# Kernel optimization log

Hardware: AMD Instinct MI355X
Metric: run time of the kernel (lower is better)

## Reference

```python
import jax, jax.numpy as jnp
import numpy as np

H = 32        # num query heads
KVH = 8       # num kv heads (GQA)
D = 128       # head_size
DV = 128      # head_size_v
SCALE = 0.08838834764831845  # 1/sqrt(128)


def setup_inputs() -> dict:
    key = jax.random.key(0)
    k1, k2, k3 = jax.random.split(key, 3)
    T = 4096  # packed tokens: B=4 sequences of seq_len=1024
    return {
        "query": jax.random.normal(k1, (T, H * D), dtype=jnp.float32),
        "key": jax.random.normal(k2, (T, KVH * D), dtype=jnp.float32),
        "value": jax.random.normal(k3, (T, KVH * DV), dtype=jnp.float32),
        "seq_len": 1024,
    }


def reference(query, key, value, seq_len):
    # Packed varlen causal GQA attention: tokens [T, H*D] split into B
    # sequences of length seq_len, causal mask within each sequence.
    T = query.shape[0]
    B = T // seq_len
    G = H // KVH  # GQA group size

    q = query.reshape(B, seq_len, H, D)
    k = key.reshape(B, seq_len, KVH, D)
    v = value.reshape(B, seq_len, KVH, DV)

    # expand kv heads to match query heads (head i uses kv head i // G)
    k = jnp.repeat(k, G, axis=2)  # [B, S, H, D]
    v = jnp.repeat(v, G, axis=2)  # [B, S, H, DV]

    scores = jnp.einsum("bqhd,bkhd->bhqk", q, k) * SCALE  # [B, H, S, S]
    causal = jnp.tril(jnp.ones((seq_len, seq_len), dtype=bool))
    scores = jnp.where(causal[None, None], scores, jnp.finfo(scores.dtype).min)
    probs = jax.nn.softmax(scores, axis=-1)
    out = jnp.einsum("bhqk,bkhd->bqhd", probs, v)  # [B, S, H, DV]
    return out.reshape(T, H * DV)
```

## Files before the change

### kernel.cpp

```cpp
#include <hip/hip_runtime.h>
#include <hip/hip_bf16.h>

#define H_   32
#define KVH_ 8
#define D_   128
#define DV_  128
#define SEQ_ 1024
#define QKD  (H_*D_)
#define KVD  (KVH_*D_)
#define CS_  (0.08838834764831845f * 1.4426950408889634f)
#define MFIX 8.0f
#define VOFF 8388608

typedef __attribute__((ext_vector_type(8))) short bf16x8;
typedef __attribute__((ext_vector_type(8))) unsigned short u16x8;
typedef __attribute__((ext_vector_type(4))) float f32x4;
typedef __attribute__((ext_vector_type(4))) unsigned int u32x4;

typedef const __attribute__((address_space(1))) void* gp_t;
typedef __attribute__((address_space(3))) void* lp_t;

#if __has_builtin(__builtin_amdgcn_exp2f)
#define EXP2F(x) __builtin_amdgcn_exp2f(x)
#else
#define EXP2F(x) exp2f(x)
#endif

static __device__ __forceinline__ unsigned short f2b(float x) {
    __hip_bfloat16 b = __float2bfloat16(x);
    return __builtin_bit_cast(unsigned short, b);
}
static __device__ __forceinline__ unsigned pk2(float a, float b) {
    return (unsigned)f2b(a) | ((unsigned)f2b(b) << 16);
}

__global__ __launch_bounds__(256)
void prep_kv(const float* __restrict__ K, const float* __restrict__ V,
             unsigned short* __restrict__ Kb, unsigned short* __restrict__ Vt) {
    if (blockIdx.x < 2048) {
        const int gt = blockIdx.x * 256 + threadIdx.x;
        const int q  = gt & 15;
        const int r  = gt >> 4;
        const int s  = r & 1023;
        const int bh = r >> 10;
        const int b = bh >> 3, kvh = bh & 7;
        const float* src = K + ((size_t)(b * SEQ_ + s)) * KVD + kvh * D_ + q * 8;
        float4 a = *(const float4*)src;
        float4 c = *(const float4*)(src + 4);
        u32x4 o = { pk2(a.x, a.y), pk2(a.z, a.w), pk2(c.x, c.y), pk2(c.z, c.w) };
        *(u32x4*)(Kb + (size_t)r * 128 + q * 8) = o;
    } else {
        const int gt = (blockIdx.x - 2048) * 256 + threadIdx.x;
        const int dv = gt & 127;
        const int uc = (gt >> 7) & 127;
        const int bh = gt >> 14;
        const int b = bh >> 3, kvh = bh & 7;
        const int C  = uc * 8;
        const int t  = C >> 5;
        const float* src = V + ((size_t)(b * SEQ_)) * KVD + kvh * DV_ + dv;
        unsigned short e[8];
#pragma unroll
        for (int i = 0; i < 8; ++i) {
            const int c = (C & 31) + i;
            const int kl = 4 * ((c >> 3) & 3) + (c & 3) + 16 * ((c >> 2) & 1);
            const int s = (t << 5) + kl;
            e[i] = f2b(src[(size_t)s * KVD]);
        }
        u16x8 o = { e[0], e[1], e[2], e[3], e[4], e[5], e[6], e[7] };
        *(u16x8*)(Vt + ((size_t)bh * 128 + dv) * SEQ_ + C) = o;
    }
}

__global__ __launch_bounds__(512, 4)
void attn_fwd(const float* __restrict__ Q,
              const unsigned short* __restrict__ Kb,
              float* __restrict__ O) {
    __shared__ __align__(16) unsigned short KS[2][32 * 128];
    __shared__ __align__(16) unsigned short VT[2][128 * 32];

    const int raw = (int)blockIdx.x;
    const int qt  = 7 - (raw >> 7);
    const int low = raw & 127;
    const int kvh = low & 7;
    const int hq  = (low >> 3) & 3;
    const int b   = low >> 5;
    const int h   = kvh * 4 + hq;
    const int bh  = b * 8 + kvh;

    const int tid = threadIdx.x;
    const int w   = tid >> 6;
    const int l   = tid & 63;
    const int lo  = l & 15;
    const int g   = l >> 4;

    const int kr = tid >> 4, ks = tid & 15;
    const int offk = kr * 256 + (((ks & 8) | ((ks & 7) ^ (kr & 7))) << 4);
    const int offv = VOFF + (tid >> 2) * 2048 + (((tid & 3) ^ ((tid >> 3) & 3)) << 4);

    const char* base = (const char*)Kb + (size_t)bh * 262144;

    auto issue = [&](int t, int dsel) {
        char* ksd = (char*)KS[dsel] + w * 1024;
        char* vsd = (char*)VT[dsel] + w * 1024;
        __builtin_amdgcn_global_load_lds((gp_t)(base + (size_t)(offk + t * 8192)), (lp_t)ksd, 16, 0, 0);
        __builtin_amdgcn_global_load_lds((gp_t)(base + (size_t)(offv + t * 64)),   (lp_t)vsd, 16, 0, 0);
    };

    const int ntiles = 4 * qt + 4;
    const int qw0    = qt * 128 + w * 16;
    const int jmaxw  = (qw0 + 15) >> 5;

    const float* Qb = Q + ((size_t)(b * SEQ_ + qw0 + lo)) * QKD + h * D_;
    bf16x8 qf[4];
#pragma unroll
    for (int cc = 0; cc < 4; ++cc) {
        const float* qp = Qb + cc * 32 + g * 8;
        float4 x0 = *(const float4*)(qp);
        float4 x1 = *(const float4*)(qp + 4);
        bf16x8 f;
        f[0] = f2b(x0.x * CS_); f[1] = f2b(x0.y * CS_);
        f[2] = f2b(x0.z * CS_); f[3] = f2b(x0.w * CS_);
        f[4] = f2b(x1.x * CS_); f[5] = f2b(x1.y * CS_);
        f[6] = f2b(x1.z * CS_); f[7] = f2b(x1.w * CS_);
        qf[cc] = f;
    }

    float lsum = 0.f;
    f32x4 o_[8];
#pragma unroll
    for (int db = 0; db < 8; ++db) o_[db] = (f32x4){0.f, 0.f, 0.f, 0.f};

    issue(0, 0);

#pragma unroll 1
    for (int j = 0; j < ntiles; ++j) {
        __syncthreads();
        if (j + 1 < ntiles) issue(j + 1, (j + 1) & 1);
        if (j <= jmaxw) {
            const int k0 = j * 32;
            const int d  = j & 1;

            f32x4 s0 = (f32x4){0.f, 0.f, 0.f, 0.f};
            f32x4 s1 = (f32x4){0.f, 0.f, 0.f, 0.f};
            const int sw = (lo & 7) << 4;
            const char* kbase = (const char*)KS[d];
            __builtin_amdgcn_s_setprio(1);
#pragma unroll
            for (int cc = 0; cc < 4; ++cc) {
                bf16x8 kf0 = *(const bf16x8*)(kbase + ((lo * 256 + cc * 64 + g * 16) ^ sw));
                bf16x8 kf1 = *(const bf16x8*)(kbase + (((16 + lo) * 256 + cc * 64 + g * 16) ^ sw));
                s0 = __builtin_amdgcn_mfma_f32_16x16x32_bf16(kf0, qf[cc], s0, 0, 0, 0);
                s1 = __builtin_amdgcn_mfma_f32_16x16x32_bf16(kf1, qf[cc], s1, 0, 0, 0);
            }
            __builtin_amdgcn_s_setprio(0);

            const int q_  = qw0 + lo;
            const bool needmask = (k0 + 31) > qw0;
            float pp[8];
#pragma unroll
            for (int i = 0; i < 4; ++i) {
                float v0 = s0[i], v1 = s1[i];
                if (needmask) {
                    if (k0 + 4 * g + i > q_)      v0 = -INFINITY;
                    if (k0 + 16 + 4 * g + i > q_) v1 = -INFINITY;
                }
                pp[i]     = EXP2F(v0 - MFIX);
                pp[4 + i] = EXP2F(v1 - MFIX);
            }
            lsum += ((pp[0] + pp[1]) + (pp[2] + pp[3]))
                  + ((pp[4] + pp[5]) + (pp[6] + pp[7]));
            u32x4 pu = { pk2(pp[0], pp[1]), pk2(pp[2], pp[3]),
                         pk2(pp[4], pp[5]), pk2(pp[6], pp[7]) };
            bf16x8 pf = __builtin_bit_cast(bf16x8, pu);

            const char* vbase = (const char*)VT[d];
            const int swv = ((lo >> 1) & 3) << 4;
            __builtin_amdgcn_s_setprio(1);
#pragma unroll
            for (int db = 0; db < 8; ++db) {
                bf16x8 vf = *(const bf16x8*)(vbase + (db * 16 + lo) * 64 + ((g * 16) ^ swv));
                o_[db] = __builtin_amdgcn_mfma_f32_16x16x32_bf16(pf, vf, o_[db], 0, 0, 0);
            }
            __builtin_amdgcn_s_setprio(0);
        }
    }

    float rs = lsum;
    rs += __shfl_xor(rs, 16);
    rs += __shfl_xor(rs, 32);
#pragma unroll
    for (int i = 0; i < 4; ++i) {
        const float inv = 1.0f / __shfl(rs, 4 * g + i);
        float* op = O + ((size_t)(b * SEQ_ + qw0 + 4 * g + i)) * (H_ * DV_) + h * DV_ + lo;
#pragma unroll
        for (int db = 0; db < 8; ++db) op[db * 16] = o_[db][i] * inv;
    }
}

extern "C" void kernel_launch(void* const* d_in, const int* in_sizes, int n_in,
                              void* d_out, int out_size, void* d_ws, size_t ws_size,
                              hipStream_t stream) {
    const float* Q = (const float*)d_in[0];
    const float* K = (const float*)d_in[1];
    const float* V = (const float*)d_in[2];
    float* Out = (float*)d_out;
    unsigned short* Kb = (unsigned short*)d_ws;
    unsigned short* Vt = (unsigned short*)((char*)d_ws + VOFF);
    prep_kv<<<dim3(4096), dim3(256), 0, stream>>>(K, V, Kb, Vt);
    attn_fwd<<<dim3(1024), dim3(512), 0, stream>>>(Q, Kb, Out);
}
```

Baseline: 72.05 us.

## Double KV tile to 64 keys per iteration to halve barrier count

Each main-loop iteration now stages 64 keys of K and V into LDS instead of 32, and processes them as two 32-key sub-tiles. This halves the number of __syncthreads and async-load rounds per block, with a new V swizzle matching the wider row. LDS use doubles to 64 KB per block and the occupancy hint of 4 blocks is dropped, so fewer blocks may be resident per CU.

```diff
diff --git a/kernel.cpp b/kernel.cpp
--- a/kernel.cpp
+++ b/kernel.cpp
@@ -71,12 +71,12 @@
     }
 }
 
-__global__ __launch_bounds__(512, 4)
+__global__ __launch_bounds__(512)
 void attn_fwd(const float* __restrict__ Q,
               const unsigned short* __restrict__ Kb,
               float* __restrict__ O) {
-    __shared__ __align__(16) unsigned short KS[2][32 * 128];
-    __shared__ __align__(16) unsigned short VT[2][128 * 32];
+    __shared__ __align__(16) unsigned short KS[2][64 * 128];
+    __shared__ __align__(16) unsigned short VT[2][128 * 64];
 
     const int raw = (int)blockIdx.x;
     const int qt  = 7 - (raw >> 7);
@@ -93,22 +93,30 @@
     const int lo  = l & 15;
     const int g   = l >> 4;
 
-    const int kr = tid >> 4, ks = tid & 15;
-    const int offk = kr * 256 + (((ks & 8) | ((ks & 7) ^ (kr & 7))) << 4);
-    const int offv = VOFF + (tid >> 2) * 2048 + (((tid & 3) ^ ((tid >> 3) & 3)) << 4);
+    const int kr0 = tid >> 4, ks0 = tid & 15;
+    const int kr1 = kr0 + 32;
+    const int offk0 = kr0 * 256 + (((ks0 & 8) | ((ks0 & 7) ^ (kr0 & 7))) << 4);
+    const int offk1 = kr1 * 256 + (((ks0 & 8) | ((ks0 & 7) ^ (kr1 & 7))) << 4);
+    const int dv0 = tid >> 3, vi = tid & 7;
+    const int offv0 = VOFF + dv0 * 2048 + ((vi ^ (dv0 & 7)) << 4);
+    const int offv1 = VOFF + (dv0 + 64) * 2048 + ((vi ^ (dv0 & 7)) << 4);
 
     const char* base = (const char*)Kb + (size_t)bh * 262144;
 
     auto issue = [&](int t, int dsel) {
         char* ksd = (char*)KS[dsel] + w * 1024;
         char* vsd = (char*)VT[dsel] + w * 1024;
-        __builtin_amdgcn_global_load_lds((gp_t)(base + (size_t)(offk + t * 8192)), (lp_t)ksd, 16, 0, 0);
-        __builtin_amdgcn_global_load_lds((gp_t)(base + (size_t)(offv + t * 64)),   (lp_t)vsd, 16, 0, 0);
+        const int ko = t * 16384;
+        const int vo = t * 128;
+        __builtin_amdgcn_global_load_lds((gp_t)(base + (size_t)(offk0 + ko)), (lp_t)ksd,          16, 0, 0);
+        __builtin_amdgcn_global_load_lds((gp_t)(base + (size_t)(offk1 + ko)), (lp_t)(ksd + 8192), 16, 0, 0);
+        __builtin_amdgcn_global_load_lds((gp_t)(base + (size_t)(offv0 + vo)), (lp_t)vsd,          16, 0, 0);
+        __builtin_amdgcn_global_load_lds((gp_t)(base + (size_t)(offv1 + vo)), (lp_t)(vsd + 8192), 16, 0, 0);
     };
 
-    const int ntiles = 4 * qt + 4;
+    const int ntiles = 2 * qt + 2;
     const int qw0    = qt * 128 + w * 16;
-    const int jmaxw  = (qw0 + 15) >> 5;
+    const int jmaxw  = (qw0 + 15) >> 6;
 
     const float* Qb = Q + ((size_t)(b * SEQ_ + qw0 + lo)) * QKD + h * D_;
     bf16x8 qf[4];
@@ -137,51 +145,56 @@
         __syncthreads();
         if (j + 1 < ntiles) issue(j + 1, (j + 1) & 1);
         if (j <= jmaxw) {
-            const int k0 = j * 32;
-            const int d  = j & 1;
-
-            f32x4 s0 = (f32x4){0.f, 0.f, 0.f, 0.f};
-            f32x4 s1 = (f32x4){0.f, 0.f, 0.f, 0.f};
+            const int d = j & 1;
+            const char* kbase = (const char*)KS[d];
+            const char* vbase = (const char*)VT[d];
             const int sw = (lo & 7) << 4;
-            const char* kbase = (const char*)KS[d];
-            __builtin_amdgcn_s_setprio(1);
-#pragma unroll
-            for (int cc = 0; cc < 4; ++cc) {
-                bf16x8 kf0 = *(const bf16x8*)(kbase + ((lo * 256 + cc * 64 + g * 16) ^ sw));
-                bf16x8 kf1 = *(const bf16x8*)(kbase + (((16 + lo) * 256 + cc * 64 + g * 16) ^ sw));
-                s0 = __builtin_amdgcn_mfma_f32_16x16x32_bf16(kf0, qf[cc], s0, 0, 0, 0);
-                s1 = __builtin_amdgcn_mfma_f32_16x16x32_bf16(kf1, qf[cc], s1, 0, 0, 0);
+
+#pragma unroll
+            for (int sub = 0; sub < 2; ++sub) {
+                const int k0 = j * 64 + sub * 32;
+                if (k0 > qw0 + 15) continue;
+
+                f32x4 s0 = (f32x4){0.f, 0.f, 0.f, 0.f};
+                f32x4 s1 = (f32x4){0.f, 0.f, 0.f, 0.f};
+                const int krow = sub * 32;
+                __builtin_amdgcn_s_setprio(1);
+#pragma unroll
+                for (int cc = 0; cc < 4; ++cc) {
+                    bf16x8 kf0 = *(const bf16x8*)(kbase + (((krow + lo) * 256 + cc * 64 + g * 16) ^ sw));
+                    bf16x8 kf1 = *(const bf16x8*)(kbase + (((krow + 16 + lo) * 256 + cc * 64 + g * 16) ^ sw));
+                    s0 = __builtin_amdgcn_mfma_f32_16x16x32_bf16(kf0, qf[cc], s0, 0, 0, 0);
+                    s1 = __builtin_amdgcn_mfma_f32_16x16x32_bf16(kf1, qf[cc], s1, 0, 0, 0);
+                }
+                __builtin_amdgcn_s_setprio(0);
+
+                const int q_  = qw0 + lo;
+                const bool needmask = (k0 + 31) > qw0;
+                float pp[8];
+#pragma unroll
+                for (int i = 0; i < 4; ++i) {
+                    float v0 = s0[i], v1 = s1[i];
+                    if (needmask) {
+                        if (k0 + 4 * g + i > q_)      v0 = -INFINITY;
+                        if (k0 + 16 + 4 * g + i > q_) v1 = -INFINITY;
+                    }
+                    pp[i]     = EXP2F(v0 - MFIX);
+                    pp[4 + i] = EXP2F(v1 - MFIX);
+                }
+                lsum += ((pp[0] + pp[1]) + (pp[2] + pp[3]))
+                      + ((pp[4] + pp[5]) + (pp[6] + pp[7]));
+                u32x4 pu = { pk2(pp[0], pp[1]), pk2(pp[2], pp[3]),
+                             pk2(pp[4], pp[5]), pk2(pp[6], pp[7]) };
+                bf16x8 pf = __builtin_bit_cast(bf16x8, pu);
+
+                __builtin_amdgcn_s_setprio(1);
+#pragma unroll
+                for (int db = 0; db < 8; ++db) {
+                    bf16x8 vf = *(const bf16x8*)(vbase + (db * 16 + lo) * 128 + ((sub * 64 + g * 16) ^ sw));
+                    o_[db] = __builtin_amdgcn_mfma_f32_16x16x32_bf16(pf, vf, o_[db], 0, 0, 0);
+                }
+                __builtin_amdgcn_s_setprio(0);
             }
-            __builtin_amdgcn_s_setprio(0);
-
-            const int q_  = qw0 + lo;
-            const bool needmask = (k0 + 31) > qw0;
-            float pp[8];
-#pragma unroll
-            for (int i = 0; i < 4; ++i) {
-                float v0 = s0[i], v1 = s1[i];
-                if (needmask) {
-                    if (k0 + 4 * g + i > q_)      v0 = -INFINITY;
-                    if (k0 + 16 + 4 * g + i > q_) v1 = -INFINITY;
-                }
-                pp[i]     = EXP2F(v0 - MFIX);
-                pp[4 + i] = EXP2F(v1 - MFIX);
-            }
-            lsum += ((pp[0] + pp[1]) + (pp[2] + pp[3]))
-                  + ((pp[4] + pp[5]) + (pp[6] + pp[7]));
-            u32x4 pu = { pk2(pp[0], pp[1]), pk2(pp[2], pp[3]),
-                         pk2(pp[4], pp[5]), pk2(pp[6], pp[7]) };
-            bf16x8 pf = __builtin_bit_cast(bf16x8, pu);
-
-            const char* vbase = (const char*)VT[d];
-            const int swv = ((lo >> 1) & 3) << 4;
-            __builtin_amdgcn_s_setprio(1);
-#pragma unroll
-            for (int db = 0; db < 8; ++db) {
-                bf16x8 vf = *(const bf16x8*)(vbase + (db * 16 + lo) * 64 + ((g * 16) ^ swv));
-                o_[db] = __builtin_amdgcn_mfma_f32_16x16x32_bf16(pf, vf, o_[db], 0, 0, 0);
-            }
-            __builtin_amdgcn_s_setprio(0);
         }
     }
 
```

Measured after the change: 71.15 us. About the same (-1.2%).

## Switch attention to 32x32x16 MFMA with 4-wave blocks and pre-swizzled KV

Applied to the files above, without the earlier changes.

Reworks the attention kernel so each wave handles 32 query rows using 32x32x16 bf16 MFMA instead of 16x16x32, and halves the block to 256 threads. The KV prep kernel now writes K and V already in the swizzled tile order the kernel reads, so tile loads become contiguous global-to-LDS copies. v_permlane32_swap rearranges the probability fragments for the PV product. This aims to reduce LDS reads and instruction count per FLOP, at the cost of more accumulator registers per lane and coarser causal-mask granularity per wave.

```diff
diff --git a/kernel.cpp b/kernel.cpp
--- a/kernel.cpp
+++ b/kernel.cpp
@@ -12,10 +12,10 @@
 #define MFIX 8.0f
 #define VOFF 8388608
 
-typedef __attribute__((ext_vector_type(8))) short bf16x8;
-typedef __attribute__((ext_vector_type(8))) unsigned short u16x8;
-typedef __attribute__((ext_vector_type(4))) float f32x4;
-typedef __attribute__((ext_vector_type(4))) unsigned int u32x4;
+typedef __attribute__((ext_vector_type(8)))  short bf16x8;
+typedef __attribute__((ext_vector_type(4)))  float f32x4;
+typedef __attribute__((ext_vector_type(16))) float f32x16;
+typedef __attribute__((ext_vector_type(4)))  unsigned int u32x4;
 
 typedef const __attribute__((address_space(1))) void* gp_t;
 typedef __attribute__((address_space(3))) void* lp_t;
@@ -38,45 +38,49 @@
 void prep_kv(const float* __restrict__ K, const float* __restrict__ V,
              unsigned short* __restrict__ Kb, unsigned short* __restrict__ Vt) {
     if (blockIdx.x < 2048) {
-        const int gt = blockIdx.x * 256 + threadIdx.x;
-        const int q  = gt & 15;
-        const int r  = gt >> 4;
-        const int s  = r & 1023;
-        const int bh = r >> 10;
+        const int gt  = blockIdx.x * 256 + threadIdx.x;
+        const int bh  = gt >> 14;
+        const int rem = gt & 16383;
+        const int j   = rem >> 9;
+        const int r   = (rem >> 4) & 31;
+        const int ust = rem & 15;
+        const int ulg = ust ^ (r & 7) ^ (((r >> 3) & 1) << 3);
         const int b = bh >> 3, kvh = bh & 7;
-        const float* src = K + ((size_t)(b * SEQ_ + s)) * KVD + kvh * D_ + q * 8;
+        const float* src = K + ((size_t)(b * SEQ_ + j * 32 + r)) * KVD + kvh * D_ + ulg * 8;
         float4 a = *(const float4*)src;
         float4 c = *(const float4*)(src + 4);
         u32x4 o = { pk2(a.x, a.y), pk2(a.z, a.w), pk2(c.x, c.y), pk2(c.z, c.w) };
-        *(u32x4*)(Kb + (size_t)r * 128 + q * 8) = o;
+        *(u32x4*)(Kb + (size_t)gt * 8) = o;
     } else {
-        const int gt = (blockIdx.x - 2048) * 256 + threadIdx.x;
-        const int dv = gt & 127;
-        const int uc = (gt >> 7) & 127;
-        const int bh = gt >> 14;
+        const int gt  = (blockIdx.x - 2048) * 256 + threadIdx.x;
+        const int bh  = gt >> 14;
+        const int rem = gt & 16383;
+        const int j   = rem >> 9;
+        const int p   = (rem >> 3) & 63;
+        const int ust = rem & 7;
+        const int ulg = ust ^ (p & 7);
+        const int c   = ulg >> 1;
+        const int par = ulg & 1;
+        const int dv  = 2 * p + par;
         const int b = bh >> 3, kvh = bh & 7;
-        const int C  = uc * 8;
-        const int t  = C >> 5;
-        const float* src = V + ((size_t)(b * SEQ_)) * KVD + kvh * DV_ + dv;
+        const float* src = V + ((size_t)(b * SEQ_ + j * 32 + 8 * c)) * KVD + kvh * DV_ + dv;
         unsigned short e[8];
 #pragma unroll
-        for (int i = 0; i < 8; ++i) {
-            const int c = (C & 31) + i;
-            const int kl = 4 * ((c >> 3) & 3) + (c & 3) + 16 * ((c >> 2) & 1);
-            const int s = (t << 5) + kl;
-            e[i] = f2b(src[(size_t)s * KVD]);
-        }
-        u16x8 o = { e[0], e[1], e[2], e[3], e[4], e[5], e[6], e[7] };
-        *(u16x8*)(Vt + ((size_t)bh * 128 + dv) * SEQ_ + C) = o;
-    }
-}
-
-__global__ __launch_bounds__(512, 4)
+        for (int i = 0; i < 8; ++i) e[i] = f2b(src[(size_t)i * KVD]);
+        u32x4 o = { (unsigned)e[0] | ((unsigned)e[1] << 16),
+                    (unsigned)e[2] | ((unsigned)e[3] << 16),
+                    (unsigned)e[4] | ((unsigned)e[5] << 16),
+                    (unsigned)e[6] | ((unsigned)e[7] << 16) };
+        *(u32x4*)(Vt + (size_t)gt * 8) = o;
+    }
+}
+
+__global__ __launch_bounds__(256)
 void attn_fwd(const float* __restrict__ Q,
               const unsigned short* __restrict__ Kb,
               float* __restrict__ O) {
     __shared__ __align__(16) unsigned short KS[2][32 * 128];
-    __shared__ __align__(16) unsigned short VT[2][128 * 32];
+    __shared__ __align__(16) unsigned short VT[2][64 * 64];
 
     const int raw = (int)blockIdx.x;
     const int qt  = 7 - (raw >> 7);
@@ -90,47 +94,53 @@
     const int tid = threadIdx.x;
     const int w   = tid >> 6;
     const int l   = tid & 63;
-    const int lo  = l & 15;
-    const int g   = l >> 4;
-
-    const int kr = tid >> 4, ks = tid & 15;
-    const int offk = kr * 256 + (((ks & 8) | ((ks & 7) ^ (kr & 7))) << 4);
-    const int offv = VOFF + (tid >> 2) * 2048 + (((tid & 3) ^ ((tid >> 3) & 3)) << 4);
+    const int q32 = l & 31;
+    const int hh  = l >> 5;
 
     const char* base = (const char*)Kb + (size_t)bh * 262144;
 
+    const int soff = w * 2048 + l * 16;
     auto issue = [&](int t, int dsel) {
-        char* ksd = (char*)KS[dsel] + w * 1024;
-        char* vsd = (char*)VT[dsel] + w * 1024;
-        __builtin_amdgcn_global_load_lds((gp_t)(base + (size_t)(offk + t * 8192)), (lp_t)ksd, 16, 0, 0);
-        __builtin_amdgcn_global_load_lds((gp_t)(base + (size_t)(offv + t * 64)),   (lp_t)vsd, 16, 0, 0);
+        char* ksd = (char*)KS[dsel] + w * 2048;
+        char* vsd = (char*)VT[dsel] + w * 2048;
+        const char* ksrc = base + (size_t)(t * 8192 + soff);
+        const char* vsrc = base + (size_t)(VOFF + t * 8192 + soff);
+        __builtin_amdgcn_global_load_lds((gp_t)ksrc,          (lp_t)ksd,          16, 0, 0);
+        __builtin_amdgcn_global_load_lds((gp_t)(ksrc + 1024), (lp_t)(ksd + 1024), 16, 0, 0);
+        __builtin_amdgcn_global_load_lds((gp_t)vsrc,          (lp_t)vsd,          16, 0, 0);
+        __builtin_amdgcn_global_load_lds((gp_t)(vsrc + 1024), (lp_t)(vsd + 1024), 16, 0, 0);
     };
 
     const int ntiles = 4 * qt + 4;
-    const int qw0    = qt * 128 + w * 16;
-    const int jmaxw  = (qw0 + 15) >> 5;
-
-    const float* Qb = Q + ((size_t)(b * SEQ_ + qw0 + lo)) * QKD + h * D_;
-    bf16x8 qf[4];
-#pragma unroll
-    for (int cc = 0; cc < 4; ++cc) {
-        const float* qp = Qb + cc * 32 + g * 8;
-        float4 x0 = *(const float4*)(qp);
-        float4 x1 = *(const float4*)(qp + 4);
-        bf16x8 f;
-        f[0] = f2b(x0.x * CS_); f[1] = f2b(x0.y * CS_);
-        f[2] = f2b(x0.z * CS_); f[3] = f2b(x0.w * CS_);
-        f[4] = f2b(x1.x * CS_); f[5] = f2b(x1.y * CS_);
-        f[6] = f2b(x1.z * CS_); f[7] = f2b(x1.w * CS_);
-        qf[cc] = f;
+    const int qw0    = qt * 128 + w * 32;
+    const int jmaxw  = (qw0 + 31) >> 5;
+
+    bf16x8 qf[8];
+    {
+        const float* Qr = Q + ((size_t)(b * SEQ_ + qw0 + q32)) * QKD + h * D_ + 8 * hh;
+#pragma unroll
+        for (int s = 0; s < 8; ++s) {
+            const float* qp = Qr + 16 * s;
+            float4 x0 = *(const float4*)(qp);
+            float4 x1 = *(const float4*)(qp + 4);
+            bf16x8 f;
+            f[0] = f2b(x0.x * CS_); f[1] = f2b(x0.y * CS_);
+            f[2] = f2b(x0.z * CS_); f[3] = f2b(x0.w * CS_);
+            f[4] = f2b(x1.x * CS_); f[5] = f2b(x1.y * CS_);
+            f[6] = f2b(x1.z * CS_); f[7] = f2b(x1.w * CS_);
+            qf[s] = f;
+        }
     }
 
     float lsum = 0.f;
-    f32x4 o_[8];
-#pragma unroll
-    for (int db = 0; db < 8; ++db) o_[db] = (f32x4){0.f, 0.f, 0.f, 0.f};
+    f32x16 o_[4];
+#pragma unroll
+    for (int nn = 0; nn < 4; ++nn) o_[nn] = (f32x16)(0.f);
 
     issue(0, 0);
+
+    const int ksw = ((q32 & 7) << 4) ^ (((q32 >> 3) & 1) << 7);
+    const int vsw = (((q32 >> 1) & 7) << 4);
 
 #pragma unroll 1
     for (int j = 0; j < ntiles; ++j) {
@@ -139,61 +149,79 @@
         if (j <= jmaxw) {
             const int k0 = j * 32;
             const int d  = j & 1;
-
-            f32x4 s0 = (f32x4){0.f, 0.f, 0.f, 0.f};
-            f32x4 s1 = (f32x4){0.f, 0.f, 0.f, 0.f};
-            const int sw = (lo & 7) << 4;
             const char* kbase = (const char*)KS[d];
+            const char* vbase = (const char*)VT[d];
+
+            f32x16 sacc = (f32x16)(0.f);
             __builtin_amdgcn_s_setprio(1);
 #pragma unroll
-            for (int cc = 0; cc < 4; ++cc) {
-                bf16x8 kf0 = *(const bf16x8*)(kbase + ((lo * 256 + cc * 64 + g * 16) ^ sw));
-                bf16x8 kf1 = *(const bf16x8*)(kbase + (((16 + lo) * 256 + cc * 64 + g * 16) ^ sw));
-                s0 = __builtin_amdgcn_mfma_f32_16x16x32_bf16(kf0, qf[cc], s0, 0, 0, 0);
-                s1 = __builtin_amdgcn_mfma_f32_16x16x32_bf16(kf1, qf[cc], s1, 0, 0, 0);
+            for (int s = 0; s < 8; ++s) {
+                bf16x8 kf = *(const bf16x8*)(kbase + q32 * 256 + (((hh + 2 * s) << 4) ^ ksw));
+                sacc = __builtin_amdgcn_mfma_f32_32x32x16_bf16(kf, qf[s], sacc, 0, 0, 0);
             }
             __builtin_amdgcn_s_setprio(0);
 
-            const int q_  = qw0 + lo;
+            const int qglob = qw0 + q32;
             const bool needmask = (k0 + 31) > qw0;
-            float pp[8];
-#pragma unroll
-            for (int i = 0; i < 4; ++i) {
-                float v0 = s0[i], v1 = s1[i];
-                if (needmask) {
-                    if (k0 + 4 * g + i > q_)      v0 = -INFINITY;
-                    if (k0 + 16 + 4 * g + i > q_) v1 = -INFINITY;
+            unsigned um[8];
+            float rsum = 0.f;
+#pragma unroll
+            for (int m = 0; m < 4; ++m) {
+                float p_[4];
+#pragma unroll
+                for (int i = 0; i < 4; ++i) {
+                    float v = sacc[4 * m + i];
+                    if (needmask) {
+                        const int kg = k0 + 8 * m + 4 * hh + i;
+                        if (kg > qglob) v = -INFINITY;
+                    }
+                    p_[i] = EXP2F(v - MFIX);
                 }
-                pp[i]     = EXP2F(v0 - MFIX);
-                pp[4 + i] = EXP2F(v1 - MFIX);
+                rsum += (p_[0] + p_[1]) + (p_[2] + p_[3]);
+                um[2 * m]     = pk2(p_[0], p_[1]);
+                um[2 * m + 1] = pk2(p_[2], p_[3]);
             }
-            lsum += ((pp[0] + pp[1]) + (pp[2] + pp[3]))
-                  + ((pp[4] + pp[5]) + (pp[6] + pp[7]));
-            u32x4 pu = { pk2(pp[0], pp[1]), pk2(pp[2], pp[3]),
-                         pk2(pp[4], pp[5]), pk2(pp[6], pp[7]) };
-            bf16x8 pf = __builtin_bit_cast(bf16x8, pu);
-
-            const char* vbase = (const char*)VT[d];
-            const int swv = ((lo >> 1) & 3) << 4;
+            lsum += rsum;
+            asm volatile("s_nop 3\n\tv_permlane32_swap_b32 %0, %1" : "+v"(um[0]), "+v"(um[2]));
+            asm volatile("s_nop 3\n\tv_permlane32_swap_b32 %0, %1" : "+v"(um[1]), "+v"(um[3]));
+            asm volatile("s_nop 3\n\tv_permlane32_swap_b32 %0, %1" : "+v"(um[4]), "+v"(um[6]));
+            asm volatile("s_nop 3\n\tv_permlane32_swap_b32 %0, %1" : "+v"(um[5]), "+v"(um[7]));
+            u32x4 pa0 = { um[0], um[1], um[2], um[3] };
+            u32x4 pa1 = { um[4], um[5], um[6], um[7] };
+            bf16x8 pf0 = __builtin_bit_cast(bf16x8, pa0);
+            bf16x8 pf1 = __builtin_bit_cast(bf16x8, pa1);
+
             __builtin_amdgcn_s_setprio(1);
 #pragma unroll
-            for (int db = 0; db < 8; ++db) {
-                bf16x8 vf = *(const bf16x8*)(vbase + (db * 16 + lo) * 64 + ((g * 16) ^ swv));
-                o_[db] = __builtin_amdgcn_mfma_f32_16x16x32_bf16(pf, vf, o_[db], 0, 0, 0);
+            for (int nn = 0; nn < 4; ++nn) {
+                const int prow = (32 * nn + q32) >> 1;
+                const int parb = (q32 & 1);
+                bf16x8 vf0 = *(const bf16x8*)(vbase + prow * 128 +
+                               (((((hh) << 1) | parb) << 4) ^ vsw));
+                bf16x8 vf1 = *(const bf16x8*)(vbase + prow * 128 +
+                               (((((hh + 2) << 1) | parb) << 4) ^ vsw));
+                o_[nn] = __builtin_amdgcn_mfma_f32_32x32x16_bf16(pf0, vf0, o_[nn], 0, 0, 0);
+                o_[nn] = __builtin_amdgcn_mfma_f32_32x32x16_bf16(pf1, vf1, o_[nn], 0, 0, 0);
             }
             __builtin_amdgcn_s_setprio(0);
         }
     }
 
-    float rs = lsum;
-    rs += __shfl_xor(rs, 16);
-    rs += __shfl_xor(rs, 32);
-#pragma unroll
-    for (int i = 0; i < 4; ++i) {
-        const float inv = 1.0f / __shfl(rs, 4 * g + i);
-        float* op = O + ((size_t)(b * SEQ_ + qw0 + 4 * g + i)) * (H_ * DV_) + h * DV_ + lo;
-#pragma unroll
-        for (int db = 0; db < 8; ++db) op[db * 16] = o_[db][i] * inv;
+    float rs = lsum + __shfl_xor(lsum, 32);
+    float inv[16];
+#pragma unroll
+    for (int r = 0; r < 16; ++r) {
+        const int qr = (r & 3) + 8 * (r >> 2) + 4 * hh;
+        inv[r] = 1.0f / __shfl(rs, qr);
+    }
+#pragma unroll
+    for (int nn = 0; nn < 4; ++nn) {
+#pragma unroll
+        for (int r = 0; r < 16; ++r) {
+            const int qr = (r & 3) + 8 * (r >> 2) + 4 * hh;
+            float* op = O + ((size_t)(b * SEQ_ + qw0 + qr)) * (H_ * DV_) + h * DV_ + 32 * nn + q32;
+            *op = o_[nn][r] * inv[r];
+        }
     }
 }
 
@@ -207,5 +235,5 @@
     unsigned short* Kb = (unsigned short*)d_ws;
     unsigned short* Vt = (unsigned short*)((char*)d_ws + VOFF);
     prep_kv<<<dim3(4096), dim3(256), 0, stream>>>(K, V, Kb, Vt);
-    attn_fwd<<<dim3(1024), dim3(512), 0, stream>>>(Q, Kb, Out);
-}
+    attn_fwd<<<dim3(1024), dim3(256), 0, stream>>>(Q, Kb, Out);
+}
```

Result: slower. 89.43 us (+24.1%).
